# Performance work log

Hardware: AMD Instinct MI355X
Metric: run time of the kernel (lower is better)

The kernel has to match this reference:

```python
import jax, jax.numpy as jnp
import numpy as np

SCALE = 64.0
MARGIN = 0.35
EPS = 1e-12  # torch F.normalize eps


def _l2norm(a, axis):
    n = jnp.sqrt(jnp.sum(a * a, axis=axis, keepdims=True))
    return a / jnp.maximum(n, EPS)


def setup_inputs() -> dict:
    key = jax.random.key(0)
    k1, k2, k3 = jax.random.split(key, 3)
    B, D, C = 512, 512, 100000
    x = jax.random.normal(k1, (B, D), dtype=jnp.float32)
    gt = jax.random.randint(k2, (B,), 0, C, dtype=jnp.int64)
    # kaiming_normal_ on [C, D]: std = sqrt(2 / fan_in) with fan_in = D
    wt = jax.random.normal(k3, (C, D), dtype=jnp.float32) * np.sqrt(2.0 / D)
    return {"x": x, "gt": gt, "wt": wt}


def reference(x, gt, wt):
    wt_norm = _l2norm(wt, axis=1)          # [C, D]
    x_norm = _l2norm(x, axis=1)            # [B, D]
    cos = jnp.einsum("bd,cd->bc", x_norm, wt_norm)  # [B, C]
    # margin only at target index (avoids materializing one-hot)
    b = jnp.arange(x.shape[0])
    margin_score = cos.at[b, gt].add(-MARGIN)
    logits = SCALE * margin_score
    logp = jax.nn.log_softmax(logits, axis=-1)
    nll = -logp[b, gt]
    return jnp.mean(nll)
```

## Files before the change

kernel.cpp:

```cpp
#include <hip/hip_runtime.h>
#include <hip/hip_bf16.h>

#define DIM 512
#define BATCH 512
#define CCLS 100000
#define BM 256
#define BN 128
#define NT 782

typedef __attribute__((ext_vector_type(4))) float f32x4;
typedef __attribute__((ext_vector_type(4))) int i32x4;
typedef __attribute__((ext_vector_type(8))) int i32x8;

__device__ __forceinline__ void async_copy16(const unsigned char* g, unsigned char* l) {
  __builtin_amdgcn_global_load_lds((const __attribute__((address_space(1))) void*)g,
                                   (__attribute__((address_space(3))) void*)l, 16, 0, 0);
}

__global__ __launch_bounds__(256) void rownorm_fp8(const float* __restrict__ wt,
                                                   const float* __restrict__ x,
                                                   unsigned char* __restrict__ wn,
                                                   unsigned char* __restrict__ xn) {
  int wave = threadIdx.x >> 6;
  int lane = threadIdx.x & 63;
  int row4 = blockIdx.x * 4 + wave;
  const float* in;
  unsigned char* out;
  int row;
  if (row4 < CCLS) { in = wt; out = wn; row = row4; }
  else             { in = x;  out = xn; row = row4 - CCLS; }
  const float4* src = (const float4*)(in + (size_t)row * DIM);
  float4 v0 = src[2 * lane];
  float4 v1 = src[2 * lane + 1];
  float ss = v0.x*v0.x + v0.y*v0.y + v0.z*v0.z + v0.w*v0.w
           + v1.x*v1.x + v1.y*v1.y + v1.z*v1.z + v1.w*v1.w;
  #pragma unroll
  for (int off = 32; off > 0; off >>= 1) ss += __shfl_xor(ss, off, 64);
  float r = 1.0f / fmaxf(sqrtf(ss), 1e-12f);
  int p0 = __builtin_amdgcn_cvt_pk_fp8_f32(v0.x * r, v0.y * r, 0, false);
  p0     = __builtin_amdgcn_cvt_pk_fp8_f32(v0.z * r, v0.w * r, p0, true);
  int p1 = __builtin_amdgcn_cvt_pk_fp8_f32(v1.x * r, v1.y * r, 0, false);
  p1     = __builtin_amdgcn_cvt_pk_fp8_f32(v1.z * r, v1.w * r, p1, true);
  ((int2*)(out + (size_t)row * DIM))[lane] = make_int2(p0, p1);
}

__global__ __launch_bounds__(512, 2) void cosface_gemm(
    const unsigned char* __restrict__ xn,
    const unsigned char* __restrict__ wn,
    const int* __restrict__ gt,
    float* __restrict__ partial,
    float* __restrict__ tgt) {
  __shared__ __align__(16) unsigned char lds_a[BM * 128];
  __shared__ __align__(16) unsigned char lds_b[BN * 128];
  __shared__ float lds_rowsum[BM];
  __shared__ int lds_gt[BM];

  const int tid = threadIdx.x;
  const int lane = tid & 63;
  const int w = tid >> 6;
  const int wm = w >> 1;
  const int wn_ = w & 1;
  const int mt = blockIdx.x;
  const int nt = blockIdx.y;

  if (tid < BM) {
    lds_rowsum[tid] = 0.f;
    lds_gt[tid] = gt[mt * BM + tid];
  }

  unsigned int oa[4];
  unsigned int ob[2];
  #pragma unroll
  for (int j = 0; j < 4; ++j) {
    int c = j * 512 + tid;
    int m = c >> 3;
    int qg = (c & 7) ^ (m & 7);
    oa[j] = (unsigned int)(mt * BM + m) * DIM + qg * 16;
  }
  #pragma unroll
  for (int j = 0; j < 2; ++j) {
    int c = j * 512 + tid;
    int m = c >> 3;
    int qg = (c & 7) ^ (m & 7);
    int rowB = nt * BN + m;
    if (rowB >= CCLS) rowB = CCLS - 1;
    ob[j] = (unsigned int)rowB * DIM + qg * 16;
  }

  f32x4 acc[4][4];
  #pragma unroll
  for (int i = 0; i < 4; ++i)
    #pragma unroll
    for (int j = 0; j < 4; ++j)
      acc[i][j] = (f32x4){0.f, 0.f, 0.f, 0.f};

  const int quad = lane >> 4;
  const int l15 = lane & 15;
  const int arow = wm * 64 + l15;
  const int brow = wn_ * 64 + l15;
  const int swA = arow & 7;
  const int swB = brow & 7;
  const int c0 = quad * 2;
  const int c1 = quad * 2 + 1;

  for (int kk = 0; kk < 4; ++kk) {
    #pragma unroll
    for (int j = 0; j < 4; ++j)
      async_copy16(xn + oa[j] + kk * 128, &lds_a[(j * 512 + w * 64) * 16]);
    #pragma unroll
    for (int j = 0; j < 2; ++j)
      async_copy16(wn + ob[j] + kk * 128, &lds_b[(j * 512 + w * 64) * 16]);
    __syncthreads();

    i32x8 af[4];
    #pragma unroll
    for (int i = 0; i < 4; ++i) {
      const unsigned char* pa = &lds_a[(arow + i * 16) * 128];
      i32x4 lo = *(const i32x4*)(pa + ((c0 ^ swA) << 4));
      i32x4 hi = *(const i32x4*)(pa + ((c1 ^ swA) << 4));
      af[i] = __builtin_shufflevector(lo, hi, 0, 1, 2, 3, 4, 5, 6, 7);
    }
    #pragma unroll
    for (int j = 0; j < 4; ++j) {
      const unsigned char* pb = &lds_b[(brow + j * 16) * 128];
      i32x4 lo = *(const i32x4*)(pb + ((c0 ^ swB) << 4));
      i32x4 hi = *(const i32x4*)(pb + ((c1 ^ swB) << 4));
      i32x8 bf = __builtin_shufflevector(lo, hi, 0, 1, 2, 3, 4, 5, 6, 7);
      #pragma unroll
      for (int i = 0; i < 4; ++i)
        acc[i][j] = __builtin_amdgcn_mfma_scale_f32_16x16x128_f8f6f4(
            af[i], bf, acc[i][j], 0, 0, 0, 127, 0, 127);
    }
    __syncthreads();
  }

  #pragma unroll
  for (int i = 0; i < 4; ++i) {
    #pragma unroll
    for (int reg = 0; reg < 4; ++reg) {
      int m_loc = wm * 64 + i * 16 + quad * 4 + reg;
      int m_g = mt * BM + m_loc;
      int gtm = lds_gt[m_loc];
      float s = 0.f;
      #pragma unroll
      for (int j = 0; j < 4; ++j) {
        int n_g = nt * BN + wn_ * 64 + j * 16 + l15;
        float logit = 64.f * acc[i][j][reg];
        if (n_g == gtm) {
          logit -= 64.f * 0.35f;
          tgt[m_g] = logit;
        }
        if (n_g < CCLS) s += __expf(logit - 64.f);
      }
      #pragma unroll
      for (int off = 1; off < 16; off <<= 1) s += __shfl_xor(s, off, 64);
      if (l15 == 0) atomicAdd(&lds_rowsum[m_loc], s);
    }
  }
  __syncthreads();
  if (tid < BM)
    partial[(size_t)(mt * BM + tid) * NT + nt] = lds_rowsum[tid];
}

__global__ __launch_bounds__(64) void nll_rows(const float* __restrict__ partial,
                                               const float* __restrict__ tgt,
                                               float* __restrict__ nll) {
  int m = blockIdx.x;
  int lane = threadIdx.x;
  const float* row = partial + (size_t)m * NT;
  float s = 0.f;
  for (int t = lane; t < NT; t += 64) s += row[t];
  #pragma unroll
  for (int off = 32; off > 0; off >>= 1) s += __shfl_xor(s, off, 64);
  if (lane == 0) nll[m] = (logf(s) + 64.f) - tgt[m];
}

__global__ __launch_bounds__(512) void reduce_mean(const float* __restrict__ nll,
                                                   float* __restrict__ out) {
  __shared__ float red[BATCH];
  int m = threadIdx.x;
  red[m] = nll[m];
  __syncthreads();
  for (int k = 256; k > 0; k >>= 1) {
    if (m < k) red[m] += red[m + k];
    __syncthreads();
  }
  if (m == 0) out[0] = red[0] * (1.0f / BATCH);
}

extern "C" void kernel_launch(void* const* d_in, const int* in_sizes, int n_in,
                              void* d_out, int out_size, void* d_ws, size_t ws_size,
                              hipStream_t stream) {
  const float* x  = (const float*)d_in[0];
  const int*   gt = (const int*)d_in[1];
  const float* wt = (const float*)d_in[2];
  float* out = (float*)d_out;

  char* ws = (char*)d_ws;
  unsigned char* wn = (unsigned char*)ws;
  unsigned char* xn = (unsigned char*)(ws + 51200000);
  float* partial    = (float*)(ws + 51462144);
  float* tgt        = (float*)(ws + 53063680);
  float* nll        = (float*)(ws + 53065728);

  rownorm_fp8<<<(CCLS + BATCH) / 4, 256, 0, stream>>>(wt, x, wn, xn);
  cosface_gemm<<<dim3(2, NT), 512, 0, stream>>>(xn, wn, gt, partial, tgt);
  nll_rows<<<BATCH, 64, 0, stream>>>(partial, tgt, nll);
  reduce_mean<<<1, BATCH, 0, stream>>>(nll, out);
}
```

Measured before the change: 376.9 us.

## Double-buffer LDS tiles in cosface GEMM to overlap loads with MFMA

Adds two-stage LDS buffers for the A and B tiles, so the async global-to-LDS copy for the next K slice is issued before the current slice's MFMAs run. One barrier per iteration replaces two, waiting on vmcnt(0) before it. The aim is to hide global load latency behind compute, at the cost of doubling LDS use (about 96KB per block with launch bounds of 2 blocks per CU), which may reduce occupancy.

```diff
diff --git a/kernel.cpp b/kernel.cpp
--- a/kernel.cpp
+++ b/kernel.cpp
@@ -50,8 +50,8 @@
     const int* __restrict__ gt,
     float* __restrict__ partial,
     float* __restrict__ tgt) {
-  __shared__ __align__(16) unsigned char lds_a[BM * 128];
-  __shared__ __align__(16) unsigned char lds_b[BN * 128];
+  __shared__ __align__(16) unsigned char lds_a[2][BM * 128];
+  __shared__ __align__(16) unsigned char lds_b[2][BN * 128];
   __shared__ float lds_rowsum[BM];
   __shared__ int lds_gt[BM];
 
@@ -86,6 +86,15 @@
     if (rowB >= CCLS) rowB = CCLS - 1;
     ob[j] = (unsigned int)rowB * DIM + qg * 16;
   }
+
+#define STAGE(sel, kk) do {                                                  \
+    _Pragma("unroll")                                                        \
+    for (int j = 0; j < 4; ++j)                                              \
+      async_copy16(xn + oa[j] + (kk) * 128, &lds_a[sel][(j * 512 + w * 64) * 16]); \
+    _Pragma("unroll")                                                        \
+    for (int j = 0; j < 2; ++j)                                              \
+      async_copy16(wn + ob[j] + (kk) * 128, &lds_b[sel][(j * 512 + w * 64) * 16]); \
+  } while (0)
 
   f32x4 acc[4][4];
   #pragma unroll
@@ -103,26 +112,25 @@
   const int c0 = quad * 2;
   const int c1 = quad * 2 + 1;
 
+  STAGE(0, 0);
+  __syncthreads();
+
+  #pragma unroll
   for (int kk = 0; kk < 4; ++kk) {
-    #pragma unroll
-    for (int j = 0; j < 4; ++j)
-      async_copy16(xn + oa[j] + kk * 128, &lds_a[(j * 512 + w * 64) * 16]);
-    #pragma unroll
-    for (int j = 0; j < 2; ++j)
-      async_copy16(wn + ob[j] + kk * 128, &lds_b[(j * 512 + w * 64) * 16]);
-    __syncthreads();
+    const int cur = kk & 1;
+    if (kk < 3) STAGE(cur ^ 1, kk + 1);
 
     i32x8 af[4];
     #pragma unroll
     for (int i = 0; i < 4; ++i) {
-      const unsigned char* pa = &lds_a[(arow + i * 16) * 128];
+      const unsigned char* pa = &lds_a[cur][(arow + i * 16) * 128];
       i32x4 lo = *(const i32x4*)(pa + ((c0 ^ swA) << 4));
       i32x4 hi = *(const i32x4*)(pa + ((c1 ^ swA) << 4));
       af[i] = __builtin_shufflevector(lo, hi, 0, 1, 2, 3, 4, 5, 6, 7);
     }
     #pragma unroll
     for (int j = 0; j < 4; ++j) {
-      const unsigned char* pb = &lds_b[(brow + j * 16) * 128];
+      const unsigned char* pb = &lds_b[cur][(brow + j * 16) * 128];
       i32x4 lo = *(const i32x4*)(pb + ((c0 ^ swB) << 4));
       i32x4 hi = *(const i32x4*)(pb + ((c1 ^ swB) << 4));
       i32x8 bf = __builtin_shufflevector(lo, hi, 0, 1, 2, 3, 4, 5, 6, 7);
@@ -131,8 +139,14 @@
         acc[i][j] = __builtin_amdgcn_mfma_scale_f32_16x16x128_f8f6f4(
             af[i], bf, acc[i][j], 0, 0, 0, 127, 0, 127);
     }
-    __syncthreads();
-  }
+
+    if (kk < 3) {
+      asm volatile("s_waitcnt vmcnt(0)" ::: "memory");
+      __builtin_amdgcn_s_barrier();
+      asm volatile("" ::: "memory");
+    }
+  }
+#undef STAGE
 
   #pragma unroll
   for (int i = 0; i < 4; ++i) {
```

New measurement: 361.9 us. 1.04x faster.
